# Kernel tuning notes

Hardware: AMD Instinct MI355X
Metric: run time of the kernel (lower is better)

Reference implementation:

```python
import jax, jax.numpy as jnp
import numpy as np

N = 100000
E = 1600000
IN_C = 256
HID = 256
OUT_C = 10
G = 64  # number of graphs in batch


def setup_inputs() -> dict:
    key = jax.random.key(0)
    k1, k2, k3, k4, k5, k6, k7 = jax.random.split(key, 7)
    x = jax.random.normal(k1, (N, IN_C), dtype=jnp.float32)
    edge_index = jax.random.randint(k2, (2, E), 0, N, dtype=jnp.int64)
    batch = jnp.sort(jax.random.randint(k3, (N,), 0, G, dtype=jnp.int64))
    # GCNConv weight (glorot-ish) and bias
    W1 = jax.random.normal(k4, (IN_C, HID), dtype=jnp.float32) / np.sqrt(IN_C)
    b1 = jnp.zeros((HID,), dtype=jnp.float32)
    # final Linear
    W2 = jax.random.normal(k5, (HID, OUT_C), dtype=jnp.float32) / np.sqrt(HID)
    b2 = jax.random.normal(k6, (OUT_C,), dtype=jnp.float32) * 0.01
    return {"x": x, "edge_index": edge_index, "batch": batch,
            "W1": W1, "b1": b1, "W2": W2, "b2": b2}


def reference(x, edge_index, batch, W1, b1, W2, b2):
    # ---- GCNConv(in_channels, hidden_dim), add_self_loops=True, symmetric norm ----
    src = edge_index[0]
    dst = edge_index[1]
    loop = jnp.arange(N, dtype=src.dtype)
    src = jnp.concatenate([src, loop])  # [E+N]
    dst = jnp.concatenate([dst, loop])
    # degree on destination nodes (incl. self-loops) -> >= 1 everywhere
    deg = jax.ops.segment_sum(jnp.ones_like(dst, dtype=x.dtype), dst, num_segments=N)
    dinv = jax.lax.rsqrt(deg)  # deg >= 1, safe
    h = x @ W1  # linear transform first (PyG GCNConv order)
    norm = dinv[src] * dinv[dst]  # [E+N]
    msgs = h[src] * norm[:, None]  # gather + scale
    agg = jax.ops.segment_sum(msgs, dst, num_segments=N) + b1  # scatter-add + bias
    # ---- relu; dropout is identity in eval mode ----
    hrelu = jax.nn.relu(agg)
    # ---- global_mean_pool over batch ids ----
    sums = jax.ops.segment_sum(hrelu, batch, num_segments=G)
    counts = jax.ops.segment_sum(jnp.ones((N,), dtype=x.dtype), batch, num_segments=G)
    pooled = sums / jnp.maximum(counts, 1.0)[:, None]  # [G, HID]
    # ---- final linear ----
    return pooled @ W2 + b2
```

## Files before the change

kernel.cpp:

```cpp
#include <hip/hip_runtime.h>

#define NN 100000
#define EE 1600000
#define C 256
#define OUTC 10
#define NG 64

#define NBK 391
#define CHUNK 2048
#define NBLK1 ((EE + CHUNK - 1) / CHUNK)
#define PADSLACK 2304

#define NODES_PER_GROUP 8
#define NODES_PER_BLOCK 32

typedef __bf16 bf16x8 __attribute__((ext_vector_type(8)));
typedef float f32x4 __attribute__((ext_vector_type(4)));
typedef float f32x2 __attribute__((ext_vector_type(2)));

__device__ __forceinline__ int chan_logical(int p) {
    return ((p & 15) << 4) | (p >> 4);
}

__device__ __forceinline__ ushort f2bf(float f) {
    unsigned u = __float_as_uint(f);
    return (ushort)((u + 0x7fffu + ((u >> 16) & 1u)) >> 16);
}
__device__ __forceinline__ bf16x8 as_bf16x8(uint4 v) {
    union { uint4 u; bf16x8 b; } c; c.u = v; return c.b;
}

__device__ __forceinline__ void acc_fp8x4(float4& s, unsigned v) {
    f32x2 lo = __builtin_amdgcn_cvt_pk_f32_fp8(v, false);
    f32x2 hi = __builtin_amdgcn_cvt_pk_f32_fp8(v, true);
    s.x += lo[0]; s.y += lo[1]; s.z += hi[0]; s.w += hi[1];
}

__global__ __launch_bounds__(1024) void count_kernel(const int* __restrict__ batch,
                                                     float* __restrict__ cnt) {
    __shared__ int h[NG];
    if (threadIdx.x < NG) h[threadIdx.x] = 0;
    __syncthreads();
    int i = blockIdx.x * blockDim.x + threadIdx.x;
    if (i < NN) atomicAdd(&h[batch[i]], 1);
    __syncthreads();
    if (threadIdx.x < NG) {
        int v = h[threadIdx.x];
        if (v > 0) atomicAdd(&cnt[threadIdx.x], (float)v);
    }
}

__global__ __launch_bounds__(256) void bucket_hist_kernel(const int* __restrict__ ei,
                                                          int* __restrict__ bhist) {
    __shared__ int h[NBK];
    for (int t = threadIdx.x; t < NBK; t += 256) h[t] = 0;
    __syncthreads();
    const int base = blockIdx.x * CHUNK;
    const int end = min(base + CHUNK, EE);
    for (int e = base + threadIdx.x; e < end; e += 256)
        atomicAdd(&h[ei[EE + e] >> 8], 1);
    __syncthreads();
    for (int t = threadIdx.x; t < NBK; t += 256)
        if (h[t]) atomicAdd(&bhist[t], h[t]);
}

__global__ __launch_bounds__(512) void bucket_scan_kernel(const int* __restrict__ bhist,
                                                          int* __restrict__ bbase,
                                                          int* __restrict__ bcur) {
    __shared__ int sc[512];
    const int t = threadIdx.x;
    int v = (t < NBK) ? bhist[t] : 0;
    sc[t] = v;
    __syncthreads();
    for (int off = 1; off < 512; off <<= 1) {
        int tmp = (t >= off) ? sc[t - off] : 0;
        __syncthreads();
        sc[t] += tmp;
        __syncthreads();
    }
    int excl = sc[t] - v;
    if (t < NBK) { bbase[t] = excl; bcur[t] = excl; }
    if (t == 0) bbase[NBK] = sc[511];
}

__global__ __launch_bounds__(256) void bucket_scatter_kernel(const int* __restrict__ ei,
                                                             int* __restrict__ bcur,
                                                             unsigned* __restrict__ bmaj) {
    __shared__ int h[NBK];
    for (int t = threadIdx.x; t < NBK; t += 256) h[t] = 0;
    __syncthreads();
    const int base = blockIdx.x * CHUNK;
    const int end = min(base + CHUNK, EE);
    for (int e = base + threadIdx.x; e < end; e += 256)
        atomicAdd(&h[ei[EE + e] >> 8], 1);
    __syncthreads();
    for (int t = threadIdx.x; t < NBK; t += 256) {
        int c = h[t];
        h[t] = c ? atomicAdd(&bcur[t], c) : 0;
    }
    __syncthreads();
    for (int e = base + threadIdx.x; e < end; e += 256) {
        int d = ei[EE + e];
        int s = ei[e];
        int b = d >> 8;
        int p = atomicAdd(&h[b], 1);
        bmaj[p] = (unsigned)s | ((unsigned)(d & 255) << 17);
    }
}

__global__ __launch_bounds__(256) void bucket_csr_kernel(const unsigned* __restrict__ bmaj,
                                                         const int* __restrict__ bbase,
                                                         int* __restrict__ rowend,
                                                         float* __restrict__ dinv,
                                                         int* __restrict__ csrcol) {
    __shared__ int h[256];
    __shared__ int sc[256];
    __shared__ int cur[256];
    const int b = blockIdx.x;
    const int t = threadIdx.x;
    const int e0 = bbase[b], e1 = bbase[b + 1];
    const int region0 = ((e0 + 7) & ~7) + b * PADSLACK;
    h[t] = 0;
    __syncthreads();
    for (int e = e0 + t; e < e1; e += 256)
        atomicAdd(&h[bmaj[e] >> 17], 1);
    __syncthreads();
    int deg = h[t];
    int node = b * 256 + t;
    int pd = (node < NN) ? ((deg + 8) & ~7) : 0;
    sc[t] = pd;
    __syncthreads();
    for (int off = 1; off < 256; off <<= 1) {
        int tmp = (t >= off) ? sc[t - off] : 0;
        __syncthreads();
        sc[t] += tmp;
        __syncthreads();
    }
    int pstart = region0 + sc[t] - pd;
    if (node < NN) {
        rowend[node] = pstart + pd;
        dinv[node] = rsqrtf((float)deg + 1.0f);
        csrcol[pstart] = node;
        for (int j = deg + 1; j < pd; j++) csrcol[pstart + j] = NN;
    }
    cur[t] = pstart + 1;
    __syncthreads();
    for (int e = e0 + t; e < e1; e += 256) {
        unsigned v = bmaj[e];
        int p = atomicAdd(&cur[v >> 17], 1);
        csrcol[p] = (int)(v & 0x1FFFFu);
    }
}

__global__ __launch_bounds__(256) void w1pack_kernel(const float* __restrict__ W1,
                                                     ushort* __restrict__ w1f,
                                                     unsigned* __restrict__ gz) {
    int t = blockIdx.x * 256 + threadIdx.x;
    if (blockIdx.x == 0 && threadIdx.x < 64) gz[threadIdx.x] = 0;
    int k = t >> 8, n = t & 255;
    int kb = k >> 5, q = (k >> 3) & 3, j = k & 7;
    int nt = n >> 4, ln = (n & 15) + q * 16;
    w1f[(size_t)(((kb * 16 + nt) * 64) + ln) * 8 + j] = f2bf(W1[t]);
}

__global__ __launch_bounds__(256) void gemm_mfma_kernel(const float* __restrict__ x,
                                                        const ushort* __restrict__ w1f,
                                                        const float* __restrict__ dinv,
                                                        uchar* __restrict__ g) {
    const int lane = threadIdx.x & 63;
    const int wid = threadIdx.x >> 6;
    const int wave = blockIdx.x * 4 + wid;
    const int r0 = wave * 32;
    if (r0 >= NN) return;
    const int mrow = lane & 15;
    const int q = lane >> 4;

    f32x4 acc[2][16];
    #pragma unroll
    for (int mt = 0; mt < 2; mt++)
        #pragma unroll
        for (int nt = 0; nt < 16; nt++)
            acc[mt][nt] = (f32x4){0.f, 0.f, 0.f, 0.f};

    const float* xp0 = x + (size_t)(r0 + mrow) * C + q * 8;
    const float* xp1 = xp0 + (size_t)16 * C;
    const ushort* bp = w1f + (size_t)lane * 8;

    #pragma unroll 1
    for (int kb = 0; kb < 8; kb++) {
        const int ko = kb * 32;
        float4 a0lo = *(const float4*)(xp0 + ko);
        float4 a0hi = *(const float4*)(xp0 + ko + 4);
        float4 a1lo = *(const float4*)(xp1 + ko);
        float4 a1hi = *(const float4*)(xp1 + ko + 4);
        bf16x8 a0, a1;
        a0[0] = (__bf16)a0lo.x; a0[1] = (__bf16)a0lo.y;
        a0[2] = (__bf16)a0lo.z; a0[3] = (__bf16)a0lo.w;
        a0[4] = (__bf16)a0hi.x; a0[5] = (__bf16)a0hi.y;
        a0[6] = (__bf16)a0hi.z; a0[7] = (__bf16)a0hi.w;
        a1[0] = (__bf16)a1lo.x; a1[1] = (__bf16)a1lo.y;
        a1[2] = (__bf16)a1lo.z; a1[3] = (__bf16)a1lo.w;
        a1[4] = (__bf16)a1hi.x; a1[5] = (__bf16)a1hi.y;
        a1[6] = (__bf16)a1hi.z; a1[7] = (__bf16)a1hi.w;

        const ushort* bkb = bp + (size_t)kb * 16 * 512;
        #pragma unroll
        for (int nt = 0; nt < 16; nt++) {
            bf16x8 bb = as_bf16x8(*(const uint4*)(bkb + (size_t)nt * 512));
            acc[0][nt] = __builtin_amdgcn_mfma_f32_16x16x32_bf16(a0, bb, acc[0][nt], 0, 0, 0);
            acc[1][nt] = __builtin_amdgcn_mfma_f32_16x16x32_bf16(a1, bb, acc[1][nt], 0, 0, 0);
        }
    }

    #pragma unroll
    for (int mt = 0; mt < 2; mt++) {
        #pragma unroll
        for (int r = 0; r < 4; r++) {
            int row = r0 + mt * 16 + q * 4 + r;
            float dv = dinv[row];
            uint4 dw;
            unsigned t0, t1, t2, t3;
            t0 = __builtin_amdgcn_cvt_pk_fp8_f32(acc[mt][0][r] * dv,  acc[mt][1][r] * dv,  0,  false);
            dw.x = __builtin_amdgcn_cvt_pk_fp8_f32(acc[mt][2][r] * dv,  acc[mt][3][r] * dv,  t0, true);
            t1 = __builtin_amdgcn_cvt_pk_fp8_f32(acc[mt][4][r] * dv,  acc[mt][5][r] * dv,  0,  false);
            dw.y = __builtin_amdgcn_cvt_pk_fp8_f32(acc[mt][6][r] * dv,  acc[mt][7][r] * dv,  t1, true);
            t2 = __builtin_amdgcn_cvt_pk_fp8_f32(acc[mt][8][r] * dv,  acc[mt][9][r] * dv,  0,  false);
            dw.z = __builtin_amdgcn_cvt_pk_fp8_f32(acc[mt][10][r] * dv, acc[mt][11][r] * dv, t2, true);
            t3 = __builtin_amdgcn_cvt_pk_fp8_f32(acc[mt][12][r] * dv, acc[mt][13][r] * dv, 0,  false);
            dw.w = __builtin_amdgcn_cvt_pk_fp8_f32(acc[mt][14][r] * dv, acc[mt][15][r] * dv, t3, true);
            *(uint4*)(g + (size_t)row * C + mrow * 16) = dw;
        }
    }
}

__global__ __launch_bounds__(256) void agg_pool_kernel(const unsigned* __restrict__ g32,
                                                       const int* __restrict__ rowend,
                                                       const int* __restrict__ csrcol,
                                                       const int* __restrict__ bbase,
                                                       const float* __restrict__ dinv,
                                                       const float* __restrict__ b1,
                                                       const int* __restrict__ batch,
                                                       float* __restrict__ sums) {
    const int lane = threadIdx.x & 63;
    const int wid = threadIdx.x >> 6;
    const int c4 = lane * 4;
    const int nodeA = blockIdx.x * NODES_PER_BLOCK + wid * NODES_PER_GROUP;
    float4 bv;
    bv.x = b1[chan_logical(c4 + 0)];
    bv.y = b1[chan_logical(c4 + 1)];
    bv.z = b1[chan_logical(c4 + 2)];
    bv.w = b1[chan_logical(c4 + 3)];
    const unsigned* gp = g32 + lane;

    int rprev;
    if ((nodeA & 255) == 0) {
        int b = nodeA >> 8;
        rprev = ((bbase[b] + 7) & ~7) + b * PADSLACK;
    } else {
        rprev = rowend[nodeA - 1];
    }

    float4 pool = make_float4(0.f, 0.f, 0.f, 0.f);
    int curb = -1;
    #pragma unroll 1
    for (int i = nodeA; i < nodeA + NODES_PER_GROUP; i++) {
        int r1 = rowend[i];
        int r0 = rprev;
        rprev = r1;
        int bi = batch[i];
        if (bi != curb) {
            if (curb >= 0) {
                atomicAdd(&sums[curb * C + c4 + 0], pool.x);
                atomicAdd(&sums[curb * C + c4 + 1], pool.y);
                atomicAdd(&sums[curb * C + c4 + 2], pool.z);
                atomicAdd(&sums[curb * C + c4 + 3], pool.w);
            }
            curb = bi;
            pool = make_float4(0.f, 0.f, 0.f, 0.f);
        }
        float4 s = make_float4(0.f, 0.f, 0.f, 0.f);
        #pragma unroll 1
        for (int e = r0; e < r1; e += 8) {
            int4 iv0 = *(const int4*)(csrcol + e);
            int4 iv1 = *(const int4*)(csrcol + e + 4);
            unsigned v0 = gp[(size_t)iv0.x * 64];
            unsigned v1 = gp[(size_t)iv0.y * 64];
            unsigned v2 = gp[(size_t)iv0.z * 64];
            unsigned v3 = gp[(size_t)iv0.w * 64];
            unsigned v4 = gp[(size_t)iv1.x * 64];
            unsigned v5 = gp[(size_t)iv1.y * 64];
            unsigned v6 = gp[(size_t)iv1.z * 64];
            unsigned v7 = gp[(size_t)iv1.w * 64];
            acc_fp8x4(s, v0); acc_fp8x4(s, v1); acc_fp8x4(s, v2); acc_fp8x4(s, v3);
            acc_fp8x4(s, v4); acc_fp8x4(s, v5); acc_fp8x4(s, v6); acc_fp8x4(s, v7);
        }
        float dv = dinv[i];
        pool.x += fmaxf(fmaf(dv, s.x, bv.x), 0.f);
        pool.y += fmaxf(fmaf(dv, s.y, bv.y), 0.f);
        pool.z += fmaxf(fmaf(dv, s.z, bv.z), 0.f);
        pool.w += fmaxf(fmaf(dv, s.w, bv.w), 0.f);
    }
    if (curb >= 0) {
        atomicAdd(&sums[curb * C + c4 + 0], pool.x);
        atomicAdd(&sums[curb * C + c4 + 1], pool.y);
        atomicAdd(&sums[curb * C + c4 + 2], pool.z);
        atomicAdd(&sums[curb * C + c4 + 3], pool.w);
    }
}

__global__ __launch_bounds__(256) void final_kernel(const float* __restrict__ sums,
                                                    const float* __restrict__ cnt,
                                                    const float* __restrict__ W2,
                                                    const float* __restrict__ b2,
                                                    float* __restrict__ out) {
    __shared__ float p[C];
    int gi = blockIdx.x;
    float cdiv = fmaxf(cnt[gi], 1.0f);
    p[threadIdx.x] = sums[gi * C + threadIdx.x] / cdiv;
    __syncthreads();
    if (threadIdx.x < OUTC) {
        float acc = b2[threadIdx.x];
        for (int k = 0; k < C; k++)
            acc += p[k] * W2[chan_logical(k) * OUTC + threadIdx.x];
        out[gi * OUTC + threadIdx.x] = acc;
    }
}

extern "C" void kernel_launch(void* const* d_in, const int* in_sizes, int n_in,
                              void* d_out, int out_size, void* d_ws, size_t ws_size,
                              hipStream_t stream) {
    const float* x     = (const float*)d_in[0];
    const int*   ei    = (const int*)d_in[1];
    const int*   batch = (const int*)d_in[2];
    const float* W1    = (const float*)d_in[3];
    const float* b1    = (const float*)d_in[4];
    const float* W2    = (const float*)d_in[5];
    const float* b2    = (const float*)d_in[6];
    float* out = (float*)d_out;

    char* w = (char*)d_ws;
    size_t off = 0;
    auto carve = [&](size_t bytes) {
        void* p = w + off;
        off = (off + bytes + 255) & ~(size_t)255;
        return p;
    };
    uchar*    g        = (uchar*)   carve((size_t)(NN + 1) * C);
    int*      rowend   = (int*)     carve((size_t)NN * 4);
    float*    dinv     = (float*)   carve((size_t)NN * 4);
    int*      csrcol   = (int*)     carve((size_t)(EE + (size_t)NBK * PADSLACK + 128) * 4);
    unsigned* bmaj     = (unsigned*)carve((size_t)EE * 4);
    int*      bbase    = (int*)     carve((size_t)(NBK + 1) * 4);
    int*      bcur     = (int*)     carve((size_t)NBK * 4);
    ushort*   w1f      = (ushort*)  carve((size_t)C * C * 2);
    int*      bhist    = (int*)     carve((size_t)NBK * 4);
    float*    sums     = (float*)   carve((size_t)NG * C * 4);
    float*    cnt      = (float*)   carve((size_t)NG * 4);
    size_t zero_bytes = (size_t)((char*)cnt + (size_t)NG * 4 - (char*)bhist);

    hipMemsetAsync(bhist, 0, zero_bytes, stream);

    bucket_hist_kernel<<<NBLK1, 256, 0, stream>>>(ei, bhist);
    bucket_scan_kernel<<<1, 512, 0, stream>>>(bhist, bbase, bcur);
    bucket_scatter_kernel<<<NBLK1, 256, 0, stream>>>(ei, bcur, bmaj);
    bucket_csr_kernel<<<NBK, 256, 0, stream>>>(bmaj, bbase, rowend, dinv, csrcol);
    count_kernel<<<(NN + 1023) / 1024, 1024, 0, stream>>>(batch, cnt);
    w1pack_kernel<<<C * C / 256, 256, 0, stream>>>(W1, w1f, (unsigned*)(g + (size_t)NN * C));
    gemm_mfma_kernel<<<(NN / 32 + 3) / 4, 256, 0, stream>>>(x, w1f, dinv, g);
    agg_pool_kernel<<<NN / NODES_PER_BLOCK, 256, 0, stream>>>(
        (const unsigned*)g, rowend, csrcol, bbase, dinv, b1, batch, sums);
    final_kernel<<<NG, 256, 0, stream>>>(sums, cnt, W2, b2, out);
}
```

Baseline: 415.3 us.

## Merge preprocessing kernels, halve bucket width, handle self-loop outside CSR, split aggregation launch

Combines the bucket histogram, batch count and W1 packing into one multi-role launch, which removes two kernel launches. Destination buckets shrink from 256 to 128 nodes, giving more CSR-building blocks and less per-bucket padding slack. The self-loop is no longer stored in the CSR and is instead added directly inside aggregation, which cuts row padding. The aggregation kernel is launched as two halves, which adds a launch but may change scheduling.

Measured after the change: 409.7 us. About the same (-1.4%).

```diff
diff --git a/kernel.cpp b/kernel.cpp
--- a/kernel.cpp
+++ b/kernel.cpp
@@ -6,13 +6,19 @@
 #define OUTC 10
 #define NG 64
 
-#define NBK 391
+#define BSH 7
+#define NBK 782
 #define CHUNK 2048
 #define NBLK1 ((EE + CHUNK - 1) / CHUNK)
-#define PADSLACK 2304
+#define PADSLACK 1024
 
 #define NODES_PER_GROUP 8
 #define NODES_PER_BLOCK 32
+#define AGG_BLOCKS 3125
+#define AGG_HALF 1563
+
+#define PRE_CNT_BLKS 391
+#define PRE_W1_BLKS 256
 
 typedef __bf16 bf16x8 __attribute__((ext_vector_type(8)));
 typedef float f32x4 __attribute__((ext_vector_type(4)));
@@ -36,43 +42,53 @@
     s.x += lo[0]; s.y += lo[1]; s.z += hi[0]; s.w += hi[1];
 }
 
-__global__ __launch_bounds__(1024) void count_kernel(const int* __restrict__ batch,
-                                                     float* __restrict__ cnt) {
-    __shared__ int h[NG];
-    if (threadIdx.x < NG) h[threadIdx.x] = 0;
-    __syncthreads();
-    int i = blockIdx.x * blockDim.x + threadIdx.x;
-    if (i < NN) atomicAdd(&h[batch[i]], 1);
-    __syncthreads();
-    if (threadIdx.x < NG) {
-        int v = h[threadIdx.x];
-        if (v > 0) atomicAdd(&cnt[threadIdx.x], (float)v);
-    }
-}
-
-__global__ __launch_bounds__(256) void bucket_hist_kernel(const int* __restrict__ ei,
-                                                          int* __restrict__ bhist) {
+__global__ __launch_bounds__(256) void pre_kernel(const int* __restrict__ ei,
+                                                  int* __restrict__ bhist,
+                                                  const int* __restrict__ batch,
+                                                  float* __restrict__ cnt,
+                                                  const float* __restrict__ W1,
+                                                  ushort* __restrict__ w1f,
+                                                  unsigned* __restrict__ gz) {
     __shared__ int h[NBK];
-    for (int t = threadIdx.x; t < NBK; t += 256) h[t] = 0;
-    __syncthreads();
-    const int base = blockIdx.x * CHUNK;
-    const int end = min(base + CHUNK, EE);
-    for (int e = base + threadIdx.x; e < end; e += 256)
-        atomicAdd(&h[ei[EE + e] >> 8], 1);
-    __syncthreads();
-    for (int t = threadIdx.x; t < NBK; t += 256)
-        if (h[t]) atomicAdd(&bhist[t], h[t]);
-}
-
-__global__ __launch_bounds__(512) void bucket_scan_kernel(const int* __restrict__ bhist,
-                                                          int* __restrict__ bbase,
-                                                          int* __restrict__ bcur) {
-    __shared__ int sc[512];
+    const int bid = blockIdx.x;
+    const int t = threadIdx.x;
+    if (bid < NBLK1) {
+        for (int i = t; i < NBK; i += 256) h[i] = 0;
+        __syncthreads();
+        const int base = bid * CHUNK;
+        const int end = min(base + CHUNK, EE);
+        for (int e = base + t; e < end; e += 256)
+            atomicAdd(&h[ei[EE + e] >> BSH], 1);
+        __syncthreads();
+        for (int i = t; i < NBK; i += 256)
+            if (h[i]) atomicAdd(&bhist[i], h[i]);
+    } else if (bid < NBLK1 + PRE_CNT_BLKS) {
+        if (t < NG) h[t] = 0;
+        __syncthreads();
+        int i = (bid - NBLK1) * 256 + t;
+        if (i < NN) atomicAdd(&h[batch[i]], 1);
+        __syncthreads();
+        if (t < NG && h[t]) atomicAdd(&cnt[t], (float)h[t]);
+    } else {
+        int wb = bid - (NBLK1 + PRE_CNT_BLKS);
+        int tt = wb * 256 + t;
+        if (wb == 0 && t < 64) gz[t] = 0;
+        int k = tt >> 8, n = tt & 255;
+        int kb = k >> 5, q = (k >> 3) & 3, j = k & 7;
+        int nt = n >> 4, ln = (n & 15) + q * 16;
+        w1f[(size_t)(((kb * 16 + nt) * 64) + ln) * 8 + j] = f2bf(W1[tt]);
+    }
+}
+
+__global__ __launch_bounds__(1024) void bucket_scan_kernel(const int* __restrict__ bhist,
+                                                           int* __restrict__ bbase,
+                                                           int* __restrict__ bcur) {
+    __shared__ int sc[1024];
     const int t = threadIdx.x;
     int v = (t < NBK) ? bhist[t] : 0;
     sc[t] = v;
     __syncthreads();
-    for (int off = 1; off < 512; off <<= 1) {
+    for (int off = 1; off < 1024; off <<= 1) {
         int tmp = (t >= off) ? sc[t - off] : 0;
         __syncthreads();
         sc[t] += tmp;
@@ -80,7 +96,7 @@
     }
     int excl = sc[t] - v;
     if (t < NBK) { bbase[t] = excl; bcur[t] = excl; }
-    if (t == 0) bbase[NBK] = sc[511];
+    if (t == NBK - 1) bbase[NBK] = sc[t];
 }
 
 __global__ __launch_bounds__(256) void bucket_scatter_kernel(const int* __restrict__ ei,
@@ -92,7 +108,7 @@
     const int base = blockIdx.x * CHUNK;
     const int end = min(base + CHUNK, EE);
     for (int e = base + threadIdx.x; e < end; e += 256)
-        atomicAdd(&h[ei[EE + e] >> 8], 1);
+        atomicAdd(&h[ei[EE + e] >> BSH], 1);
     __syncthreads();
     for (int t = threadIdx.x; t < NBK; t += 256) {
         int c = h[t];
@@ -102,9 +118,9 @@
     for (int e = base + threadIdx.x; e < end; e += 256) {
         int d = ei[EE + e];
         int s = ei[e];
-        int b = d >> 8;
+        int b = d >> BSH;
         int p = atomicAdd(&h[b], 1);
-        bmaj[p] = (unsigned)s | ((unsigned)(d & 255) << 17);
+        bmaj[p] = (unsigned)s | ((unsigned)(d & 127) << 17);
     }
 }
 
@@ -113,54 +129,47 @@
                                                          int* __restrict__ rowend,
                                                          float* __restrict__ dinv,
                                                          int* __restrict__ csrcol) {
-    __shared__ int h[256];
-    __shared__ int sc[256];
-    __shared__ int cur[256];
+    __shared__ int h[128];
+    __shared__ int sc[128];
+    __shared__ int cur[128];
     const int b = blockIdx.x;
     const int t = threadIdx.x;
     const int e0 = bbase[b], e1 = bbase[b + 1];
     const int region0 = ((e0 + 7) & ~7) + b * PADSLACK;
-    h[t] = 0;
+    if (t < 128) h[t] = 0;
     __syncthreads();
     for (int e = e0 + t; e < e1; e += 256)
         atomicAdd(&h[bmaj[e] >> 17], 1);
     __syncthreads();
-    int deg = h[t];
-    int node = b * 256 + t;
-    int pd = (node < NN) ? ((deg + 8) & ~7) : 0;
-    sc[t] = pd;
-    __syncthreads();
-    for (int off = 1; off < 256; off <<= 1) {
-        int tmp = (t >= off) ? sc[t - off] : 0;
-        __syncthreads();
-        sc[t] += tmp;
-        __syncthreads();
-    }
-    int pstart = region0 + sc[t] - pd;
-    if (node < NN) {
-        rowend[node] = pstart + pd;
-        dinv[node] = rsqrtf((float)deg + 1.0f);
-        csrcol[pstart] = node;
-        for (int j = deg + 1; j < pd; j++) csrcol[pstart + j] = NN;
-    }
-    cur[t] = pstart + 1;
+    int deg = 0, pd = 0, node = 0;
+    if (t < 128) {
+        deg = h[t];
+        node = b * 128 + t;
+        pd = (node < NN) ? ((deg + 7) & ~7) : 0;
+        sc[t] = pd;
+    }
+    __syncthreads();
+    for (int off = 1; off < 128; off <<= 1) {
+        int tmp = (t >= off && t < 128) ? sc[t - off] : 0;
+        __syncthreads();
+        if (t < 128) sc[t] += tmp;
+        __syncthreads();
+    }
+    if (t < 128) {
+        int pstart = region0 + sc[t] - pd;
+        if (node < NN) {
+            rowend[node] = pstart + pd;
+            dinv[node] = rsqrtf((float)deg + 1.0f);
+            for (int j = deg; j < pd; j++) csrcol[pstart + j] = NN;
+        }
+        cur[t] = pstart;
+    }
     __syncthreads();
     for (int e = e0 + t; e < e1; e += 256) {
         unsigned v = bmaj[e];
         int p = atomicAdd(&cur[v >> 17], 1);
         csrcol[p] = (int)(v & 0x1FFFFu);
     }
-}
-
-__global__ __launch_bounds__(256) void w1pack_kernel(const float* __restrict__ W1,
-                                                     ushort* __restrict__ w1f,
-                                                     unsigned* __restrict__ gz) {
-    int t = blockIdx.x * 256 + threadIdx.x;
-    if (blockIdx.x == 0 && threadIdx.x < 64) gz[threadIdx.x] = 0;
-    int k = t >> 8, n = t & 255;
-    int kb = k >> 5, q = (k >> 3) & 3, j = k & 7;
-    int nt = n >> 4, ln = (n & 15) + q * 16;
-    w1f[(size_t)(((kb * 16 + nt) * 64) + ln) * 8 + j] = f2bf(W1[t]);
 }
 
 __global__ __launch_bounds__(256) void gemm_mfma_kernel(const float* __restrict__ x,
@@ -240,11 +249,12 @@
                                                        const float* __restrict__ dinv,
                                                        const float* __restrict__ b1,
                                                        const int* __restrict__ batch,
-                                                       float* __restrict__ sums) {
+                                                       float* __restrict__ sums,
+                                                       const int blk0) {
     const int lane = threadIdx.x & 63;
     const int wid = threadIdx.x >> 6;
     const int c4 = lane * 4;
-    const int nodeA = blockIdx.x * NODES_PER_BLOCK + wid * NODES_PER_GROUP;
+    const int nodeA = (blockIdx.x + blk0) * NODES_PER_BLOCK + wid * NODES_PER_GROUP;
     float4 bv;
     bv.x = b1[chan_logical(c4 + 0)];
     bv.y = b1[chan_logical(c4 + 1)];
@@ -253,8 +263,8 @@
     const unsigned* gp = g32 + lane;
 
     int rprev;
-    if ((nodeA & 255) == 0) {
-        int b = nodeA >> 8;
+    if ((nodeA & 127) == 0) {
+        int b = nodeA >> BSH;
         rprev = ((bbase[b] + 7) & ~7) + b * PADSLACK;
     } else {
         rprev = rowend[nodeA - 1];
@@ -279,6 +289,7 @@
             pool = make_float4(0.f, 0.f, 0.f, 0.f);
         }
         float4 s = make_float4(0.f, 0.f, 0.f, 0.f);
+        acc_fp8x4(s, gp[(size_t)i * 64]);
         #pragma unroll 1
         for (int e = r0; e < r1; e += 8) {
             int4 iv0 = *(const int4*)(csrcol + e);
@@ -360,14 +371,15 @@
 
     hipMemsetAsync(bhist, 0, zero_bytes, stream);
 
-    bucket_hist_kernel<<<NBLK1, 256, 0, stream>>>(ei, bhist);
-    bucket_scan_kernel<<<1, 512, 0, stream>>>(bhist, bbase, bcur);
+    pre_kernel<<<NBLK1 + PRE_CNT_BLKS + PRE_W1_BLKS, 256, 0, stream>>>(
+        ei, bhist, batch, cnt, W1, w1f, (unsigned*)(g + (size_t)NN * C));
+    bucket_scan_kernel<<<1, 1024, 0, stream>>>(bhist, bbase, bcur);
     bucket_scatter_kernel<<<NBLK1, 256, 0, stream>>>(ei, bcur, bmaj);
     bucket_csr_kernel<<<NBK, 256, 0, stream>>>(bmaj, bbase, rowend, dinv, csrcol);
-    count_kernel<<<(NN + 1023) / 1024, 1024, 0, stream>>>(batch, cnt);
-    w1pack_kernel<<<C * C / 256, 256, 0, stream>>>(W1, w1f, (unsigned*)(g + (size_t)NN * C));
     gemm_mfma_kernel<<<(NN / 32 + 3) / 4, 256, 0, stream>>>(x, w1f, dinv, g);
-    agg_pool_kernel<<<NN / NODES_PER_BLOCK, 256, 0, stream>>>(
-        (const unsigned*)g, rowend, csrcol, bbase, dinv, b1, batch, sums);
+    agg_pool_kernel<<<AGG_HALF, 256, 0, stream>>>(
+        (const unsigned*)g, rowend, csrcol, bbase, dinv, b1, batch, sums, 0);
+    agg_pool_kernel<<<AGG_BLOCKS - AGG_HALF, 256, 0, stream>>>(
+        (const unsigned*)g, rowend, csrcol, bbase, dinv, b1, batch, sums, AGG_HALF);
     final_kernel<<<NG, 256, 0, stream>>>(sums, cnt, W2, b2, out);
 }
```
